# Performance work log

Hardware: AMD Instinct MI355X
Metric: run time of the kernel (lower is better)

## Reference

```python
import jax, jax.numpy as jnp
import numpy as np
from jax import lax


def ternarize(w):
    """Standard TWN ternarization with straight-through estimator.
    delta = 0.7*mean(|w|); alpha = mean(|w|) over kept entries; w_t = alpha*sign(w)*mask.
    """
    a = jnp.abs(w)
    delta = 0.7 * a.mean()
    mask = (a > delta).astype(w.dtype)
    alpha = (a * mask).sum() / jnp.maximum(mask.sum(), 1.0)
    wt = alpha * jnp.sign(w) * mask
    return w + lax.stop_gradient(wt - w)  # STE


def conv3x3(x, w, b):
    y = lax.conv_general_dilated(x, ternarize(w), window_strides=(1, 1),
                                 padding=((1, 1), (1, 1)),
                                 dimension_numbers=('NCHW', 'OIHW', 'NCHW'))
    return y + b[None, :, None, None]


def maxpool2(x):
    return lax.reduce_window(x, -jnp.inf, lax.max, (1, 1, 2, 2), (1, 1, 2, 2), 'VALID')


def setup_inputs() -> dict:
    key = jax.random.key(0)
    ks = jax.random.split(key, 11)
    s = lambda k, shape, scale: jax.random.normal(k, shape, dtype=jnp.float32) * scale
    return {
        'x':   s(ks[0], (1024, 3, 32, 32), 1.0),
        'w1':  s(ks[1], (64, 3, 3, 3), 0.1),
        'b1':  s(ks[2], (64,), 0.01),
        'w2':  s(ks[3], (128, 64, 3, 3), 0.05),
        'b2':  s(ks[4], (128,), 0.01),
        'w3':  s(ks[5], (256, 128, 3, 3), 0.03),
        'b3':  s(ks[6], (256,), 0.01),
        'wf1': s(ks[7], (256, 4096), 0.02),
        'bf1': s(ks[8], (256,), 0.01),
        'wf2': s(ks[9], (10, 256), 0.06),
        'bf2': s(ks[10], (10,), 0.01),
    }


def reference(x, w1, b1, w2, b2, w3, b3, wf1, bf1, wf2, bf2):
    x = maxpool2(jax.nn.relu(conv3x3(x, w1, b1)))   # [B,64,16,16]
    x = maxpool2(jax.nn.relu(conv3x3(x, w2, b2)))   # [B,128,8,8]
    x = maxpool2(jax.nn.relu(conv3x3(x, w3, b3)))   # [B,256,4,4]
    x = x.reshape(-1, 256 * 4 * 4)
    x = jax.nn.relu(x @ ternarize(wf1).T + bf1)     # [B,256]
    return x @ ternarize(wf2).T + bf2               # [B,10]
```

## Files before the change

### kernel.cpp

```cpp
#include <hip/hip_runtime.h>
#include <hip/hip_bf16.h>


typedef __attribute__((ext_vector_type(8))) short short8;
typedef __attribute__((ext_vector_type(4))) float f32x4;
typedef __attribute__((ext_vector_type(4))) int i32x4;

__device__ __forceinline__ unsigned short f2bf(float x) {
    unsigned u = __float_as_uint(x);
    return (unsigned short)((u + 0x7fffu + ((u >> 16) & 1u)) >> 16);
}
__device__ __forceinline__ float bf2f(unsigned short b) {
    return __uint_as_float(((unsigned)b) << 16);
}

#define WS_WT1   0
#define N_WT1    (64*3*3*3)
#define WS_W2P   (WS_WT1 + N_WT1)
#define N_W2P    (9*128*64)
#define WS_W3P   (WS_W2P + N_W2P)
#define N_W3P    (9*256*128)
#define WS_WTF1  (WS_W3P + N_W3P)
#define N_WTF1   (256*4096)
#define WS_WTF2  (WS_WTF1 + N_WTF1)
#define N_WTF2   (10*256)
#define WS_A1    (WS_WTF2 + N_WTF2)
#define N_A1     (1024*256*64)
#define WS_A2    (WS_A1 + N_A1)
#define N_A2     (1024*64*128)
#define WS_A3    (WS_A2 + N_A2)
#define N_A3     (1024*16*256)
#define WS_F1    (WS_A3 + N_A3)
#define N_F1     (1024*256)
#define WS_SCR   (WS_F1 + N_F1)

#define FC1_S    16

struct TernArgs {
    const float* w[5];
    int n[5];
};

__global__ void tern_stats1(TernArgs ta, double* __restrict__ scr) {
    const int wi = blockIdx.y;
    const float* __restrict__ w = ta.w[wi];
    const int n = ta.n[wi];
    double s = 0.0;
    for (int i = blockIdx.x * blockDim.x + threadIdx.x; i < n;
         i += gridDim.x * blockDim.x)
        s += (double)fabsf(w[i]);
    #pragma unroll
    for (int off = 32; off > 0; off >>= 1) s += __shfl_down(s, off, 64);
    __shared__ double red[4];
    const int lane = threadIdx.x & 63, wv = threadIdx.x >> 6;
    if (lane == 0) red[wv] = s;
    __syncthreads();
    if (threadIdx.x == 0)
        atomicAdd(scr + wi * 4, red[0] + red[1] + red[2] + red[3]);
}

__global__ void tern_stats2(TernArgs ta, double* __restrict__ scr) {
    const int wi = blockIdx.y;
    const float* __restrict__ w = ta.w[wi];
    const int n = ta.n[wi];
    const float delta = (float)(0.7 * scr[wi * 4] / (double)n);
    double ms = 0.0, cnt = 0.0;
    for (int i = blockIdx.x * blockDim.x + threadIdx.x; i < n;
         i += gridDim.x * blockDim.x) {
        float a = fabsf(w[i]);
        if (a > delta) { ms += (double)a; cnt += 1.0; }
    }
    #pragma unroll
    for (int off = 32; off > 0; off >>= 1) {
        ms += __shfl_down(ms, off, 64);
        cnt += __shfl_down(cnt, off, 64);
    }
    __shared__ double redm[4], redc[4];
    const int lane = threadIdx.x & 63, wv = threadIdx.x >> 6;
    if (lane == 0) { redm[wv] = ms; redc[wv] = cnt; }
    __syncthreads();
    if (threadIdx.x == 0) {
        atomicAdd(scr + wi * 4 + 1, redm[0] + redm[1] + redm[2] + redm[3]);
        atomicAdd(scr + wi * 4 + 2, redc[0] + redc[1] + redc[2] + redc[3]);
    }
}

__global__ void tern_write_all(TernArgs ta, const double* __restrict__ scr,
                               float* __restrict__ wt1,
                               signed char* __restrict__ w2p8,
                               signed char* __restrict__ w3p8,
                               unsigned short* __restrict__ wtf1b,
                               float* __restrict__ wtf2) {
    const int wi = blockIdx.y;
    const float* __restrict__ w = ta.w[wi];
    const int n = ta.n[wi];
    const double* sc = scr + wi * 4;
    const float delta = (float)(0.7 * sc[0] / (double)n);
    const int i0 = blockIdx.x * blockDim.x + threadIdx.x;
    const int stride = gridDim.x * blockDim.x;

    if (wi == 0 || wi == 4) {
        const double c = sc[2];
        const float alpha = (float)(sc[1] / (c > 1.0 ? c : 1.0));
        float* dst = (wi == 0) ? wt1 : wtf2;
        for (int i = i0; i < n; i += stride) {
            float v = w[i];
            dst[i] = (fabsf(v) > delta) ? (v > 0.0f ? alpha : -alpha) : 0.0f;
        }
    } else if (wi == 1 || wi == 2) {
        const int CIc = (wi == 1) ? 64 : 128;
        const int COc = (wi == 1) ? 128 : 256;
        signed char* dst = (wi == 1) ? w2p8 : w3p8;
        for (int i = i0; i < n; i += stride) {
            const int co = i / (CIc * 9);
            const int r = i % (CIc * 9);
            const int ci = r / 9, tap = r % 9;
            float v = w[i];
            signed char s = (fabsf(v) > delta) ? (v > 0.0f ? 1 : -1) : 0;
            dst[(tap * COc + co) * CIc + ci] = s;
        }
    } else {
        for (int i = i0; i < n; i += stride) {
            const int j = i >> 12;
            const int k = i & 4095;
            const int c = k >> 4, px = k & 15;
            float v = w[i];
            unsigned short s = (fabsf(v) > delta) ? (v > 0.0f ? 0x3f80 : 0xbf80) : 0;
            unsigned short* row = wtf1b + ((long)j << 13) + px * 512 + c;
            row[0] = s;
            row[256] = s;
        }
    }
}

__global__ __launch_bounds__(256) void conv1_q(
        const float* __restrict__ x, const float* __restrict__ wt,
        const float* __restrict__ bias, float* __restrict__ y,
        int* __restrict__ amax) {
    constexpr int HI = 32, CI = 3, CO = 64, PO = 16;
    constexpr int PP = 20;
    __shared__ float patch[CI * 18 * PP];
    __shared__ float sw[CI * 9 * CO];
    __shared__ float redm[4];

    const int b = blockIdx.x >> 2;
    const int quad = blockIdx.x & 3;
    const int tid = threadIdx.x;

    for (int i = tid; i < CO * CI * 9; i += 256) {
        const int co = i / 27;
        const int r = i % 27;
        sw[r * CO + co] = wt[i];
    }
    const int qh = (quad >> 1) * 16, qw = (quad & 1) * 16;
    for (int i = tid; i < CI * 18 * 18; i += 256) {
        const int ci = i / 324;
        const int r = (i % 324) / 18;
        const int c = i % 18;
        const int h = qh - 1 + r, w = qw - 1 + c;
        float v = 0.f;
        if ((unsigned)h < (unsigned)HI && (unsigned)w < (unsigned)HI)
            v = x[(((long)b * CI + ci) * HI + h) * HI + w];
        patch[(ci * 18 + r) * PP + c] = v;
    }
    __syncthreads();

    const int pxq = tid >> 2;
    const int cg = tid & 3;
    const int lph = pxq >> 3, lpw = pxq & 7;

    float acc[16][4];
    #pragma unroll
    for (int c = 0; c < 16; c++)
        #pragma unroll
        for (int q = 0; q < 4; q++) acc[c][q] = 0.f;

    for (int ci = 0; ci < CI; ci++) {
        float p[4][4];
        #pragma unroll
        for (int r = 0; r < 4; r++)
            #pragma unroll
            for (int c = 0; c < 4; c++)
                p[r][c] = patch[(ci * 18 + 2 * lph + r) * PP + 2 * lpw + c];
        #pragma unroll
        for (int kh = 0; kh < 3; kh++)
            #pragma unroll
            for (int kw = 0; kw < 3; kw++) {
                const float4* wv = (const float4*)
                    &sw[((ci * 3 + kh) * 3 + kw) * CO + cg * 16];
                const float4 w0 = wv[0], w1 = wv[1], w2 = wv[2], w3 = wv[3];
                const float w16[16] = {w0.x, w0.y, w0.z, w0.w,
                                       w1.x, w1.y, w1.z, w1.w,
                                       w2.x, w2.y, w2.z, w2.w,
                                       w3.x, w3.y, w3.z, w3.w};
                const float p00 = p[kh][kw], p01 = p[kh][kw + 1];
                const float p10 = p[kh + 1][kw], p11 = p[kh + 1][kw + 1];
                #pragma unroll
                for (int c = 0; c < 16; c++) {
                    const float wvv = w16[c];
                    acc[c][0] += wvv * p00;
                    acc[c][1] += wvv * p01;
                    acc[c][2] += wvv * p10;
                    acc[c][3] += wvv * p11;
                }
            }
    }

    const int gpx = ((quad >> 1) * 8 + lph) * PO + (quad & 1) * 8 + lpw;
    float* yr = y + ((long)b * 256 + gpx) * CO + cg * 16;
    float tmax = 0.f;
    #pragma unroll
    for (int c = 0; c < 16; c++) {
        float m = fmaxf(fmaxf(acc[c][0], acc[c][1]), fmaxf(acc[c][2], acc[c][3]));
        float o = fmaxf(m + bias[cg * 16 + c], 0.f);
        tmax = fmaxf(tmax, o);
        yr[c] = o;
    }
    #pragma unroll
    for (int off = 32; off > 0; off >>= 1)
        tmax = fmaxf(tmax, __shfl_down(tmax, off, 64));
    const int lane = tid & 63, wv2 = tid >> 6;
    if (lane == 0) redm[wv2] = tmax;
    __syncthreads();
    if (tid == 0) {
        float m = fmaxf(fmaxf(redm[0], redm[1]), fmaxf(redm[2], redm[3]));
        atomicMax(amax, __float_as_int(m));
    }
}

template <int CI, int HI, int CO, int HB, int WM, int WN, bool INF32>
__global__ __launch_bounds__(256) void conv_i8(
        const void* __restrict__ xin,
        const signed char* __restrict__ wp,
        const float* __restrict__ bias,
        const double* __restrict__ scr,
        const int* __restrict__ amax_in,
        int* __restrict__ amax_out,
        unsigned short* __restrict__ yout) {
    constexpr int CH8 = CI / 64;
    constexpr int NITER = 9 * CH8;
    constexpr int HR = HI / HB;
    constexpr int ROWS = HR + 2;
    constexpr int COLS = HI + 2;
    constexpr int NPIX = ROWS * COLS;
    constexpr int PSTR = NPIX * 64 + 32;
    constexpr int PO = HI / 2;
    constexpr int POR = HR / 2;
    constexpr int MT = 4, NT = 4;
    constexpr int NST = ROWS * HI * (CI / 8) / 256;
    static_assert(WM * WN == 4, "4 waves");
    static_assert(WM * 64 == HR * HI, "M covers slab pixels");
    static_assert(WN * 64 == CO, "N covers all co");
    static_assert(NST * 256 == ROWS * HI * (CI / 8), "exact staging trips");

    __shared__ __align__(16) char X[2 * CH8 * PSTR];
    __shared__ float redm[4];

    const int bimg = blockIdx.x / HB;
    const int hb = blockIdx.x % HB;
    const int tid = threadIdx.x;

    const float S = 32512.0f / fmaxf(__int_as_float(*amax_in), 1e-30f);

    constexpr int HALO = 2 * COLS + 2 * (ROWS - 2);
    for (int i = tid; i < HALO * 2 * CH8 * 4; i += 256) {
        const int u = i & 3;
        const int t = i >> 2;
        const int g = t % (2 * CH8);
        const int hp = t / (2 * CH8);
        int p;
        if (hp < COLS) p = hp;
        else if (hp < 2 * COLS) p = (ROWS - 1) * COLS + (hp - COLS);
        else {
            const int e = hp - 2 * COLS;
            p = (1 + (e >> 1)) * COLS + ((e & 1) ? (COLS - 1) : 0);
        }
        *(int4*)&X[g * PSTR + p * 64 + u * 16] = make_int4(0, 0, 0, 0);
    }

    uint4 va[NST], vb[NST];
    bool val[NST];
    int pidx[NST], cbase[NST];
    #pragma unroll
    for (int s2 = 0; s2 < NST; s2++) {
        const int i = tid + s2 * 256;
        const int q8 = i % (CI / 8);
        const int t = i / (CI / 8);
        const int c = t % HI;
        const int r = t / HI;
        const int h = hb * HR + r - 1;
        val[s2] = (unsigned)h < (unsigned)HI;
        pidx[s2] = r * COLS + c + 1;
        cbase[s2] = q8 * 8;
        if (val[s2]) {
            if (INF32) {
                const float* pxr = (const float*)xin +
                    ((long)(bimg * HI + h) * HI + c) * CI + q8 * 8;
                va[s2] = *(const uint4*)(pxr);
                vb[s2] = *(const uint4*)(pxr + 4);
            } else {
                const unsigned short* pxr = (const unsigned short*)xin +
                    ((long)(bimg * HI + h) * HI + c) * (2 * CI);
                va[s2] = *(const uint4*)(pxr + q8 * 8);
                vb[s2] = *(const uint4*)(pxr + CI + q8 * 8);
            }
        }
    }
    #pragma unroll
    for (int s2 = 0; s2 < NST; s2++) {
        if (!val[s2]) continue;
        float f[8];
        if (INF32) {
            const float* fa = (const float*)&va[s2];
            const float* fb = (const float*)&vb[s2];
            #pragma unroll
            for (int j = 0; j < 4; j++) { f[j] = fa[j]; f[4 + j] = fb[j]; }
        } else {
            const unsigned* hw = (const unsigned*)&va[s2];
            const unsigned* lw = (const unsigned*)&vb[s2];
            #pragma unroll
            for (int j = 0; j < 8; j++) {
                const unsigned hu = (j & 1) ? (hw[j >> 1] >> 16)
                                            : (hw[j >> 1] & 0xffffu);
                const unsigned lu = (j & 1) ? (lw[j >> 1] >> 16)
                                            : (lw[j >> 1] & 0xffffu);
                f[j] = __uint_as_float(hu << 16) + __uint_as_float(lu << 16);
            }
        }
        unsigned pl0 = 0, pl1 = 0, ph0 = 0, ph1 = 0;
        #pragma unroll
        for (int j = 0; j < 8; j++) {
            const int qi = (int)(f[j] * S + 0.5f);
            const int ql = (qi << 24) >> 24;
            const int qh = (qi - ql) >> 8;
            const int sh = (j & 3) * 8;
            if (j < 4) {
                pl0 |= (unsigned)(ql & 255) << sh;
                ph0 |= (unsigned)(qh & 255) << sh;
            } else {
                pl1 |= (unsigned)(ql & 255) << sh;
                ph1 |= (unsigned)(qh & 255) << sh;
            }
        }
        const int p = pidx[s2];
        const int ch = cbase[s2] >> 6;
        const int cc = cbase[s2] & 63;
        const int slot = ((cc >> 4) + (p >> 1)) & 3;
        const int base = p * 64 + slot * 16 + (cc & 15);
        *(uint2*)&X[ch * PSTR + base] = make_uint2(pl0, pl1);
        *(uint2*)&X[(CH8 + ch) * PSTR + base] = make_uint2(ph0, ph1);
    }
    __syncthreads();

    const int lane = tid & 63;
    const int wid = tid >> 6;
    const int wm = (WM == 1) ? 0 : (wid >> 1);
    const int wn = (WM == 1) ? wid : (wid & 1);
    const int lm = lane & 15;
    const int kg = lane >> 4;

    int pb[MT];
    #pragma unroll
    for (int mt = 0; mt < MT; mt++) {
        const int m = (wm * MT + mt) * 16 + lm;
        const int pp = m >> 2, sub = m & 3;
        const int lph = pp / PO, lpw = pp % PO;
        const int h = 2 * lph + (sub >> 1);
        const int w = 2 * lpw + (sub & 1);
        pb[mt] = h * COLS + w;
    }
    const signed char* bp[NT];
    #pragma unroll
    for (int nt = 0; nt < NT; nt++) {
        const int co = (wn * NT + nt) * 16 + lm;
        bp[nt] = wp + (long)co * CI + kg * 16;
    }

    i32x4 accL[MT][NT], accH[MT][NT];
    #pragma unroll
    for (int mt = 0; mt < MT; mt++)
        #pragma unroll
        for (int nt = 0; nt < NT; nt++) { accL[mt][nt] = 0; accH[mt][nt] = 0; }

    i32x4 Bb[2][NT];
    #pragma unroll
    for (int nt = 0; nt < NT; nt++) Bb[0][nt] = *(const i32x4*)(bp[nt]);

    #pragma unroll 2
    for (int it = 0; it < NITER; ++it) {
        const int cur = it & 1, nxt = cur ^ 1;
        if (it + 1 < NITER) {
            const int it1 = it + 1;
            const int tap = it1 / CH8, ch1 = it1 % CH8;
            const int woff = tap * CO * CI + ch1 * 64;
            #pragma unroll
            for (int nt = 0; nt < NT; nt++)
                Bb[nxt][nt] = *(const i32x4*)(bp[nt] + woff);
        }
        const int tap = it / CH8, ch = it % CH8;
        const int dtap = (tap / 3) * COLS + (tap % 3);
        i32x4 Af0[MT], Af1[MT];
        #pragma unroll
        for (int mt = 0; mt < MT; mt++) {
            const int p = pb[mt] + dtap;
            const int ao = p * 64 + (((kg + (p >> 1)) & 3) << 4);
            Af0[mt] = *(const i32x4*)&X[ch * PSTR + ao];
            Af1[mt] = *(const i32x4*)&X[(CH8 + ch) * PSTR + ao];
        }
        #pragma unroll
        for (int mt = 0; mt < MT; mt++)
            #pragma unroll
            for (int nt = 0; nt < NT; nt++)
                accL[mt][nt] = __builtin_amdgcn_mfma_i32_16x16x64_i8(
                    Af0[mt], Bb[cur][nt], accL[mt][nt], 0, 0, 0);
        #pragma unroll
        for (int mt = 0; mt < MT; mt++)
            #pragma unroll
            for (int nt = 0; nt < NT; nt++)
                accH[mt][nt] = __builtin_amdgcn_mfma_i32_16x16x64_i8(
                    Af1[mt], Bb[cur][nt], accH[mt][nt], 0, 0, 0);
    }

    const double c2 = scr[2];
    const float alpha = (float)(scr[1] / (c2 > 1.0 ? c2 : 1.0));
    const float dq = alpha / S;
    float tmax = 0.f;
    #pragma unroll
    for (int mt = 0; mt < MT; mt++) {
        const int pp = (wm * MT + mt) * 4 + kg;
        const int lph = pp / PO, lpw = pp % PO;
        const int gpp = (hb * POR + lph) * PO + lpw;
        unsigned short* yr = yout + ((long)bimg * (PO * PO) + gpp) * (2 * CO);
        #pragma unroll
        for (int nt = 0; nt < NT; nt++) {
            const int co = (wn * NT + nt) * 16 + lm;
            const i32x4 aL = accL[mt][nt], aH = accH[mt][nt];
            int s0 = aH[0] * 256 + aL[0];
            int s1 = aH[1] * 256 + aL[1];
            int s2 = aH[2] * 256 + aL[2];
            int s3 = aH[3] * 256 + aL[3];
            int sm = s0 > s1 ? s0 : s1;
            int sn = s2 > s3 ? s2 : s3;
            sm = sm > sn ? sm : sn;
            float o = fmaxf(dq * (float)sm + bias[co], 0.f);
            tmax = fmaxf(tmax, o);
            unsigned short hi = f2bf(o);
            unsigned short lo = f2bf(o - bf2f(hi));
            yr[co] = hi;
            yr[CO + co] = lo;
        }
    }
    if (amax_out) {
        #pragma unroll
        for (int off = 32; off > 0; off >>= 1)
            tmax = fmaxf(tmax, __shfl_down(tmax, off, 64));
        if (lane == 0) redm[wid] = tmax;
        __syncthreads();
        if (tid == 0) {
            float m = fmaxf(fmaxf(redm[0], redm[1]), fmaxf(redm[2], redm[3]));
            atomicMax(amax_out, __float_as_int(m));
        }
    }
}

template <int S>
__global__ __launch_bounds__(256) void fc1_mfma(
        const unsigned short* __restrict__ A,
        const unsigned short* __restrict__ Bw,
        float* __restrict__ parts) {
    constexpr int KCH = 8192 / S;
    constexpr int NSTEP = KCH / 32;
    const int m0 = blockIdx.x * 128;
    const int n0 = blockIdx.y * 128;
    const int s = blockIdx.z;
    const int tid = threadIdx.x;
    const int lane = tid & 63, wid = tid >> 6;
    const int wm = wid >> 1, wn = wid & 1;
    const int lm = lane & 15, kg = lane >> 4;

    const long k0 = (long)s * KCH + kg * 8;
    const unsigned short* ap[4];
    const unsigned short* bp[4];
    #pragma unroll
    for (int t = 0; t < 4; t++) {
        ap[t] = A + (long)(m0 + wm * 64 + t * 16 + lm) * 8192 + k0;
        bp[t] = Bw + (long)(n0 + wn * 64 + t * 16 + lm) * 8192 + k0;
    }

    f32x4 acc[4][4] = {};
    short8 Ab[2][4], Bb[2][4];
    #pragma unroll
    for (int t = 0; t < 4; t++) {
        Ab[0][t] = *(const short8*)(ap[t]);
        Bb[0][t] = *(const short8*)(bp[t]);
    }

    #pragma unroll 2
    for (int st = 0; st < NSTEP; ++st) {
        const int cur = st & 1, nxt = cur ^ 1;
        if (st + 1 < NSTEP) {
            const int off = (st + 1) * 32;
            #pragma unroll
            for (int t = 0; t < 4; t++) {
                Ab[nxt][t] = *(const short8*)(ap[t] + off);
                Bb[nxt][t] = *(const short8*)(bp[t] + off);
            }
        }
        #pragma unroll
        for (int mt = 0; mt < 4; mt++)
            #pragma unroll
            for (int nt = 0; nt < 4; nt++)
                acc[mt][nt] = __builtin_amdgcn_mfma_f32_16x16x32_bf16(
                    Ab[cur][mt], Bb[cur][nt], acc[mt][nt], 0, 0, 0);
    }

    #pragma unroll
    for (int mt = 0; mt < 4; mt++) {
        #pragma unroll
        for (int r = 0; r < 4; r++) {
            const int b = m0 + wm * 64 + mt * 16 + kg * 4 + r;
            #pragma unroll
            for (int nt = 0; nt < 4; nt++) {
                const int j = n0 + wn * 64 + nt * 16 + lm;
                parts[((long)s * 1024 + b) * 256 + j] = acc[mt][nt][r];
            }
        }
    }
}

template <int S>
__global__ void fc1_reduce(const float* __restrict__ parts,
                           const double* __restrict__ scr,
                           const float* __restrict__ bias,
                           float* __restrict__ f1) {
    const int idx = blockIdx.x * blockDim.x + threadIdx.x;
    const int j = idx & 255;
    float s = 0.f;
    #pragma unroll
    for (int p = 0; p < S; p++) s += parts[(long)p * 262144 + idx];
    const double c2 = scr[2];
    const float alpha = (float)(scr[1] / (c2 > 1.0 ? c2 : 1.0));
    f1[idx] = fmaxf(alpha * s + bias[j], 0.f);
}

__global__ void fc2_kernel(const float* __restrict__ a,
                           const float* __restrict__ wt,
                           const float* __restrict__ bias,
                           float* __restrict__ out, int B) {
    const int idx = blockIdx.x * blockDim.x + threadIdx.x;
    if (idx >= B * 10) return;
    const int k = idx % 10;
    const int b = idx / 10;
    const float* ar = a + (long)b * 256;
    const float* wr = wt + (long)k * 256;
    float acc = 0.f;
    #pragma unroll 4
    for (int i = 0; i < 256; i++) acc += ar[i] * wr[i];
    out[idx] = acc + bias[k];
}

extern "C" void kernel_launch(void* const* d_in, const int* in_sizes, int n_in,
                              void* d_out, int out_size, void* d_ws, size_t ws_size,
                              hipStream_t stream) {
    const float* x   = (const float*)d_in[0];
    const float* w1  = (const float*)d_in[1];
    const float* b1  = (const float*)d_in[2];
    const float* w2  = (const float*)d_in[3];
    const float* b2  = (const float*)d_in[4];
    const float* w3  = (const float*)d_in[5];
    const float* b3  = (const float*)d_in[6];
    const float* wf1 = (const float*)d_in[7];
    const float* bf1 = (const float*)d_in[8];
    const float* wf2 = (const float*)d_in[9];
    const float* bf2 = (const float*)d_in[10];
    float* out = (float*)d_out;
    float* ws = (float*)d_ws;

    const int B = 1024;

    float*          wt1   = ws + WS_WT1;
    signed char*    w2p8  = (signed char*)(ws + WS_W2P);
    signed char*    w3p8  = (signed char*)(ws + WS_W3P);
    unsigned short* wtf1b = (unsigned short*)(ws + WS_WTF1);
    float*          wtf2  = ws + WS_WTF2;
    float*          a1f   = ws + WS_A1;
    unsigned short* a2p   = (unsigned short*)(ws + WS_A2);
    unsigned short* a3p   = (unsigned short*)(ws + WS_A3);
    float*          f1    = ws + WS_F1;
    double*         scr   = (double*)(ws + WS_SCR);
    int*            amax1 = (int*)(scr + 20);
    int*            amax2 = amax1 + 1;
    float*          parts = ws + WS_A1;

    hipMemsetAsync(scr, 0, 22 * sizeof(double), stream);

    TernArgs ta;
    ta.w[0] = w1;  ta.n[0] = N_WT1;
    ta.w[1] = w2;  ta.n[1] = 128 * 64 * 9;
    ta.w[2] = w3;  ta.n[2] = 256 * 128 * 9;
    ta.w[3] = wf1; ta.n[3] = 256 * 4096;
    ta.w[4] = wf2; ta.n[4] = 10 * 256;

    hipLaunchKernelGGL(tern_stats1, dim3(128, 5), dim3(256), 0, stream, ta, scr);
    hipLaunchKernelGGL(tern_stats2, dim3(128, 5), dim3(256), 0, stream, ta, scr);
    hipLaunchKernelGGL(tern_write_all, dim3(128, 5), dim3(256), 0, stream,
                       ta, scr, wt1, w2p8, w3p8, wtf1b, wtf2);

    hipLaunchKernelGGL(conv1_q, dim3(B * 4), dim3(256), 0, stream,
                       x, wt1, b1, a1f, amax1);

    hipLaunchKernelGGL((conv_i8<64, 16, 128, 2, 2, 2, true>), dim3(B * 2),
                       dim3(256), 0, stream, a1f, w2p8, b2, scr + 4, amax1,
                       amax2, a2p);

    hipLaunchKernelGGL((conv_i8<128, 8, 256, 1, 1, 4, false>), dim3(B),
                       dim3(256), 0, stream, a2p, w3p8, b3, scr + 8, amax2,
                       (int*)nullptr, a3p);

    hipLaunchKernelGGL((fc1_mfma<FC1_S>), dim3(8, 2, FC1_S), dim3(256), 0, stream,
                       a3p, wtf1b, parts);
    hipLaunchKernelGGL((fc1_reduce<FC1_S>), dim3(1024), dim3(256), 0, stream,
                       parts, scr + 12, bf1, f1);

    hipLaunchKernelGGL(fc2_kernel, dim3((B * 10 + 255) / 256), dim3(256), 0,
                       stream, f1, wtf2, bf2, out, B);
}
```

Baseline: 323.0 us.

## Run conv1 on int8 MFMA with split-byte quantized input

New measurement: 307.8 us. 4.7% less time.

```diff
diff --git a/kernel.cpp b/kernel.cpp
--- a/kernel.cpp
+++ b/kernel.cpp
@@ -14,9 +14,9 @@
     return __uint_as_float(((unsigned)b) << 16);
 }
 
-#define WS_WT1   0
-#define N_WT1    (64*3*3*3)
-#define WS_W2P   (WS_WT1 + N_WT1)
+#define WS_W1B   0
+#define N_W1B    2048
+#define WS_W2P   (WS_W1B + N_W1B)
 #define N_W2P    (9*128*64)
 #define WS_W3P   (WS_W2P + N_W2P)
 #define N_W3P    (9*256*128)
@@ -37,22 +37,38 @@
 #define FC1_S    16
 
 struct TernArgs {
-    const float* w[5];
-    int n[5];
+    const float* w[6];
+    int n[6];
 };
 
 __global__ void tern_stats1(TernArgs ta, double* __restrict__ scr) {
     const int wi = blockIdx.y;
     const float* __restrict__ w = ta.w[wi];
     const int n = ta.n[wi];
+    __shared__ double red[4];
+    const int lane = threadIdx.x & 63, wv = threadIdx.x >> 6;
+    if (wi == 5) {
+        float m = 0.f;
+        for (int i = blockIdx.x * blockDim.x + threadIdx.x; i < n;
+             i += gridDim.x * blockDim.x)
+            m = fmaxf(m, fabsf(w[i]));
+        #pragma unroll
+        for (int off = 32; off > 0; off >>= 1)
+            m = fmaxf(m, __shfl_down(m, off, 64));
+        if (lane == 0) red[wv] = (double)m;
+        __syncthreads();
+        if (threadIdx.x == 0) {
+            float mm = (float)fmax(fmax(red[0], red[1]), fmax(red[2], red[3]));
+            atomicMax((int*)(scr + 20), __float_as_int(mm));
+        }
+        return;
+    }
     double s = 0.0;
     for (int i = blockIdx.x * blockDim.x + threadIdx.x; i < n;
          i += gridDim.x * blockDim.x)
         s += (double)fabsf(w[i]);
     #pragma unroll
     for (int off = 32; off > 0; off >>= 1) s += __shfl_down(s, off, 64);
-    __shared__ double red[4];
-    const int lane = threadIdx.x & 63, wv = threadIdx.x >> 6;
     if (lane == 0) red[wv] = s;
     __syncthreads();
     if (threadIdx.x == 0)
@@ -86,7 +102,7 @@
 }
 
 __global__ void tern_write_all(TernArgs ta, const double* __restrict__ scr,
-                               float* __restrict__ wt1,
+                               signed char* __restrict__ w1b,
                                signed char* __restrict__ w2p8,
                                signed char* __restrict__ w3p8,
                                unsigned short* __restrict__ wtf1b,
@@ -99,13 +115,21 @@
     const int i0 = blockIdx.x * blockDim.x + threadIdx.x;
     const int stride = gridDim.x * blockDim.x;
 
-    if (wi == 0 || wi == 4) {
+    if (wi == 0) {
+        for (int i = i0; i < n; i += stride) {
+            const int co = i / 27;
+            const int kp = i % 27;
+            float v = w[i];
+            signed char s = (fabsf(v) > delta) ? (v > 0.0f ? 1 : -1) : 0;
+            w1b[co * 64 + kp] = s;
+            w1b[4096 + co * 64 + 32 + kp] = s;
+        }
+    } else if (wi == 4) {
         const double c = sc[2];
         const float alpha = (float)(sc[1] / (c > 1.0 ? c : 1.0));
-        float* dst = (wi == 0) ? wt1 : wtf2;
         for (int i = i0; i < n; i += stride) {
             float v = w[i];
-            dst[i] = (fabsf(v) > delta) ? (v > 0.0f ? alpha : -alpha) : 0.0f;
+            wtf2[i] = (fabsf(v) > delta) ? (v > 0.0f ? alpha : -alpha) : 0.0f;
         }
     } else if (wi == 1 || wi == 2) {
         const int CIc = (wi == 1) ? 64 : 128;
@@ -133,98 +157,120 @@
     }
 }
 
-__global__ __launch_bounds__(256) void conv1_q(
-        const float* __restrict__ x, const float* __restrict__ wt,
-        const float* __restrict__ bias, float* __restrict__ y,
-        int* __restrict__ amax) {
-    constexpr int HI = 32, CI = 3, CO = 64, PO = 16;
-    constexpr int PP = 20;
-    __shared__ float patch[CI * 18 * PP];
-    __shared__ float sw[CI * 9 * CO];
+__global__ __launch_bounds__(256) void conv1_i8(
+        const float* __restrict__ x,
+        const signed char* __restrict__ w1b,
+        const float* __restrict__ bias,
+        const double* __restrict__ scr,
+        const int* __restrict__ amax_x,
+        int* __restrict__ amax_out,
+        float* __restrict__ y) {
+    constexpr int PL = 3472;
+    __shared__ __align__(16) char X[2 * PL];
     __shared__ float redm[4];
 
-    const int b = blockIdx.x >> 2;
-    const int quad = blockIdx.x & 3;
+    const int b = blockIdx.x;
     const int tid = threadIdx.x;
-
-    for (int i = tid; i < CO * CI * 9; i += 256) {
-        const int co = i / 27;
-        const int r = i % 27;
-        sw[r * CO + co] = wt[i];
-    }
-    const int qh = (quad >> 1) * 16, qw = (quad & 1) * 16;
-    for (int i = tid; i < CI * 18 * 18; i += 256) {
-        const int ci = i / 324;
-        const int r = (i % 324) / 18;
-        const int c = i % 18;
-        const int h = qh - 1 + r, w = qw - 1 + c;
-        float v = 0.f;
-        if ((unsigned)h < (unsigned)HI && (unsigned)w < (unsigned)HI)
-            v = x[(((long)b * CI + ci) * HI + h) * HI + w];
-        patch[(ci * 18 + r) * PP + c] = v;
-    }
+    const float S = 32512.0f / fmaxf(__int_as_float(*amax_x), 1e-30f);
+
+    for (int i = tid; i < 2 * PL / 16; i += 256)
+        ((int4*)X)[i] = make_int4(0, 0, 0, 0);
     __syncthreads();
 
-    const int pxq = tid >> 2;
-    const int cg = tid & 3;
-    const int lph = pxq >> 3, lpw = pxq & 7;
-
-    float acc[16][4];
-    #pragma unroll
-    for (int c = 0; c < 16; c++)
-        #pragma unroll
-        for (int q = 0; q < 4; q++) acc[c][q] = 0.f;
-
-    for (int ci = 0; ci < CI; ci++) {
-        float p[4][4];
-        #pragma unroll
-        for (int r = 0; r < 4; r++)
-            #pragma unroll
-            for (int c = 0; c < 4; c++)
-                p[r][c] = patch[(ci * 18 + 2 * lph + r) * PP + 2 * lpw + c];
-        #pragma unroll
-        for (int kh = 0; kh < 3; kh++)
-            #pragma unroll
-            for (int kw = 0; kw < 3; kw++) {
-                const float4* wv = (const float4*)
-                    &sw[((ci * 3 + kh) * 3 + kw) * CO + cg * 16];
-                const float4 w0 = wv[0], w1 = wv[1], w2 = wv[2], w3 = wv[3];
-                const float w16[16] = {w0.x, w0.y, w0.z, w0.w,
-                                       w1.x, w1.y, w1.z, w1.w,
-                                       w2.x, w2.y, w2.z, w2.w,
-                                       w3.x, w3.y, w3.z, w3.w};
-                const float p00 = p[kh][kw], p01 = p[kh][kw + 1];
-                const float p10 = p[kh + 1][kw], p11 = p[kh + 1][kw + 1];
-                #pragma unroll
-                for (int c = 0; c < 16; c++) {
-                    const float wvv = w16[c];
-                    acc[c][0] += wvv * p00;
-                    acc[c][1] += wvv * p01;
-                    acc[c][2] += wvv * p10;
-                    acc[c][3] += wvv * p11;
-                }
-            }
-    }
-
-    const int gpx = ((quad >> 1) * 8 + lph) * PO + (quad & 1) * 8 + lpw;
-    float* yr = y + ((long)b * 256 + gpx) * CO + cg * 16;
+    for (int i = tid; i < 768; i += 256) {
+        const float4 v = ((const float4*)(x + (long)b * 3072))[i];
+        const int e = i * 4;
+        const int ci = e >> 10;
+        const int rem = e & 1023;
+        const int h = rem >> 5, w = rem & 31;
+        const int base = ci * 1156 + (h + 1) * 34 + (w + 1);
+        const float f[4] = {v.x, v.y, v.z, v.w};
+        #pragma unroll
+        for (int j = 0; j < 4; j++) {
+            const int q = __float2int_rn(f[j] * S);
+            const int ql = (q << 24) >> 24;
+            const int qh = (q - ql) >> 8;
+            X[base + j] = (char)ql;
+            X[PL + base + j] = (char)qh;
+        }
+    }
+    __syncthreads();
+
+    const int lane = tid & 63;
+    const int wid = tid >> 6;
+    const int lm = lane & 15;
+    const int kg = lane >> 4;
+
+    const int poff = (kg >= 2) ? PL : 0;
+    int cst[16];
+    #pragma unroll
+    for (int j = 0; j < 16; j++) {
+        const int kp = (kg & 1) * 16 + j;
+        cst[j] = (kp < 27)
+                     ? ((kp / 9) * 1156 + ((kp % 9) / 3) * 34 + (kp % 9) % 3)
+                     : 0;
+    }
+
+    i32x4 BL[4], BH[4];
+    #pragma unroll
+    for (int nt = 0; nt < 4; nt++) {
+        const int co = nt * 16 + lm;
+        BL[nt] = *(const i32x4*)(w1b + (long)co * 64 + kg * 16);
+        BH[nt] = *(const i32x4*)(w1b + 4096 + (long)co * 64 + kg * 16);
+    }
+
+    const double c2 = scr[2];
+    const float alpha = (float)(scr[1] / (c2 > 1.0 ? c2 : 1.0));
+    const float dq = alpha / S;
     float tmax = 0.f;
-    #pragma unroll
-    for (int c = 0; c < 16; c++) {
-        float m = fmaxf(fmaxf(acc[c][0], acc[c][1]), fmaxf(acc[c][2], acc[c][3]));
-        float o = fmaxf(m + bias[cg * 16 + c], 0.f);
-        tmax = fmaxf(tmax, o);
-        yr[c] = o;
-    }
+    float* yb = y + (long)b * 256 * 64;
+
+    for (int tt = 0; tt < 16; ++tt) {
+        const int t = wid * 16 + tt;
+        const int pp = t * 4 + (lm >> 2);
+        const int sub = lm & 3;
+        const int h = 2 * (pp >> 4) + (sub >> 1);
+        const int w = 2 * (pp & 15) + (sub & 1);
+        const int base = poff + h * 34 + w;
+        unsigned d[4] = {0u, 0u, 0u, 0u};
+        #pragma unroll
+        for (int j = 0; j < 16; j++) {
+            const unsigned byte = (unsigned char)X[base + cst[j]];
+            d[j >> 2] |= byte << ((j & 3) * 8);
+        }
+        i32x4 Af;
+        Af[0] = (int)d[0]; Af[1] = (int)d[1];
+        Af[2] = (int)d[2]; Af[3] = (int)d[3];
+
+        const int opp = t * 4 + kg;
+        float* yr = yb + (long)opp * 64;
+        #pragma unroll
+        for (int nt = 0; nt < 4; nt++) {
+            i32x4 aL = 0, aH = 0;
+            aL = __builtin_amdgcn_mfma_i32_16x16x64_i8(Af, BL[nt], aL, 0, 0, 0);
+            aH = __builtin_amdgcn_mfma_i32_16x16x64_i8(Af, BH[nt], aH, 0, 0, 0);
+            const int s0 = aH[0] * 256 + aL[0];
+            const int s1 = aH[1] * 256 + aL[1];
+            const int s2 = aH[2] * 256 + aL[2];
+            const int s3 = aH[3] * 256 + aL[3];
+            int sm = s0 > s1 ? s0 : s1;
+            const int sn = s2 > s3 ? s2 : s3;
+            sm = sm > sn ? sm : sn;
+            const int co = nt * 16 + lm;
+            const float o = fmaxf(dq * (float)sm + bias[co], 0.f);
+            tmax = fmaxf(tmax, o);
+            yr[co] = o;
+        }
+    }
+
     #pragma unroll
     for (int off = 32; off > 0; off >>= 1)
         tmax = fmaxf(tmax, __shfl_down(tmax, off, 64));
-    const int lane = tid & 63, wv2 = tid >> 6;
-    if (lane == 0) redm[wv2] = tmax;
+    if (lane == 0) redm[wid] = tmax;
     __syncthreads();
     if (tid == 0) {
         float m = fmaxf(fmaxf(redm[0], redm[1]), fmaxf(redm[2], redm[3]));
-        atomicMax(amax, __float_as_int(m));
+        atomicMax(amax_out, __float_as_int(m));
     }
 }
 
@@ -578,7 +624,7 @@
 
     const int B = 1024;
 
-    float*          wt1   = ws + WS_WT1;
+    signed char*    w1b   = (signed char*)(ws + WS_W1B);
     signed char*    w2p8  = (signed char*)(ws + WS_W2P);
     signed char*    w3p8  = (signed char*)(ws + WS_W3P);
     unsigned short* wtf1b = (unsigned short*)(ws + WS_WTF1);
@@ -588,26 +634,30 @@
     unsigned short* a3p   = (unsigned short*)(ws + WS_A3);
     float*          f1    = ws + WS_F1;
     double*         scr   = (double*)(ws + WS_SCR);
-    int*            amax1 = (int*)(scr + 20);
-    int*            amax2 = amax1 + 1;
+    int*            iscr  = (int*)(scr + 20);
+    int*            amaxx = iscr;
+    int*            amax1 = iscr + 1;
+    int*            amax2 = iscr + 2;
     float*          parts = ws + WS_A1;
 
     hipMemsetAsync(scr, 0, 22 * sizeof(double), stream);
+    hipMemsetAsync(w1b, 0, 8192, stream);
 
     TernArgs ta;
-    ta.w[0] = w1;  ta.n[0] = N_WT1;
+    ta.w[0] = w1;  ta.n[0] = 64 * 27;
     ta.w[1] = w2;  ta.n[1] = 128 * 64 * 9;
     ta.w[2] = w3;  ta.n[2] = 256 * 128 * 9;
     ta.w[3] = wf1; ta.n[3] = 256 * 4096;
     ta.w[4] = wf2; ta.n[4] = 10 * 256;
-
-    hipLaunchKernelGGL(tern_stats1, dim3(128, 5), dim3(256), 0, stream, ta, scr);
+    ta.w[5] = x;   ta.n[5] = 1024 * 3 * 32 * 32;
+
+    hipLaunchKernelGGL(tern_stats1, dim3(128, 6), dim3(256), 0, stream, ta, scr);
     hipLaunchKernelGGL(tern_stats2, dim3(128, 5), dim3(256), 0, stream, ta, scr);
     hipLaunchKernelGGL(tern_write_all, dim3(128, 5), dim3(256), 0, stream,
-                       ta, scr, wt1, w2p8, w3p8, wtf1b, wtf2);
-
-    hipLaunchKernelGGL(conv1_q, dim3(B * 4), dim3(256), 0, stream,
-                       x, wt1, b1, a1f, amax1);
+                       ta, scr, w1b, w2p8, w3p8, wtf1b, wtf2);
+
+    hipLaunchKernelGGL(conv1_i8, dim3(B), dim3(256), 0, stream,
+                       x, w1b, b1, scr + 0, amaxx, amax1, a1f);
 
     hipLaunchKernelGGL((conv_i8<64, 16, 128, 2, 2, 2, true>), dim3(B * 2),
                        dim3(256), 0, stream, a1f, w2p8, b2, scr + 4, amax1,
```
